# Performance work log

Measured on AMD Instinct MI355X. Metric: run time of the kernel, lower is better.

## Reference

```python
import jax, jax.numpy as jnp
import numpy as np

LEAK = 0.2
NUM_GRAPHS = 64


def _gat(h_in, src, dst, eh, W, att_src, att_dst, att_edge, lin_edge_W, bias, N):
    # PyG GATConv with edge_dim, concat=False (mean over heads)
    H, C = att_src.shape
    h = (h_in @ W).reshape(N, H, C)                      # [N,H,C]
    e = (eh @ lin_edge_W).reshape(-1, H, C)              # [Eaug,H,C]
    a_s = jnp.einsum('nhc,hc->nh', h, att_src)           # [N,H]
    a_d = jnp.einsum('nhc,hc->nh', h, att_dst)
    a_e = jnp.einsum('ehc,hc->eh', e, att_edge)          # [Eaug,H]
    score = jax.nn.leaky_relu(a_s[src] + a_d[dst] + a_e, LEAK)
    # scatter-softmax over incoming edges of each destination node
    m = jax.ops.segment_max(score, dst, num_segments=N)
    ex = jnp.exp(score - m[dst])
    den = jax.ops.segment_sum(ex, dst, num_segments=N)
    alpha = ex / den[dst]                                # [Eaug,H]
    out = jax.ops.segment_sum(alpha[:, :, None] * h[src], dst, num_segments=N)
    return out.mean(axis=1) + bias                       # concat=False -> head mean


def setup_inputs() -> dict:
    key = jax.random.key(0)
    ks = jax.random.split(key, 32)
    N, E, F, FE, HID, H, NT = 30000, 480000, 64, 16, 64, 4, 16
    Cin1 = F + HID
    s = 0.05
    d = {
        'x': jax.random.normal(ks[0], (N, F), jnp.float32),
        'edge_attr': jax.random.normal(ks[1], (E, FE), jnp.float32),
        'node_emb': jax.random.normal(ks[2], (NT, HID), jnp.float32) * s,
        'edge_W': jax.random.normal(ks[3], (FE, HID), jnp.float32) * s,
        'edge_b': jnp.zeros((HID,), jnp.float32),
        'W1': jax.random.normal(ks[4], (Cin1, H * HID), jnp.float32) * s,
        'as1': jax.random.normal(ks[5], (H, HID), jnp.float32) * s,
        'ad1': jax.random.normal(ks[6], (H, HID), jnp.float32) * s,
        'ae1': jax.random.normal(ks[7], (H, HID), jnp.float32) * s,
        'leW1': jax.random.normal(ks[8], (HID, H * HID), jnp.float32) * s,
        'b1': jnp.zeros((HID,), jnp.float32),
        'W2': jax.random.normal(ks[9], (HID, H * HID), jnp.float32) * s,
        'as2': jax.random.normal(ks[10], (H, HID), jnp.float32) * s,
        'ad2': jax.random.normal(ks[11], (H, HID), jnp.float32) * s,
        'ae2': jax.random.normal(ks[12], (H, HID), jnp.float32) * s,
        'leW2': jax.random.normal(ks[13], (HID, H * HID), jnp.float32) * s,
        'b2': jnp.zeros((HID,), jnp.float32),
        'sage_Wl': jax.random.normal(ks[14], (HID, HID), jnp.float32) * s,
        'sage_bl': jnp.zeros((HID,), jnp.float32),
        'sage_Wr': jax.random.normal(ks[15], (HID, HID), jnp.float32) * s,
        'lin1_W': jax.random.normal(ks[16], (HID, HID), jnp.float32) * s,
        'lin1_b': jnp.zeros((HID,), jnp.float32),
        'lin2_W': jax.random.normal(ks[17], (HID, HID), jnp.float32) * s,
        'lin2_b': jnp.zeros((HID,), jnp.float32),
        'tel_W': jax.random.normal(ks[18], (HID, 1), jnp.float32) * s,
        'tel_b': jnp.zeros((1,), jnp.float32),
        'comp_W': jax.random.normal(ks[19], (HID, 1), jnp.float32) * s,
        'comp_b': jnp.zeros((1,), jnp.float32),
        'pch_W': jax.random.normal(ks[20], (HID, 1), jnp.float32) * s,
        'pch_b': jnp.zeros((1,), jnp.float32),
        'edge_index': jax.random.randint(ks[21], (2, E), 0, N, jnp.int32),
        'batch': jnp.sort(jax.random.randint(ks[22], (N,), 0, NUM_GRAPHS, jnp.int32)),
        'node_type': jax.random.randint(ks[23], (N,), 0, NT, jnp.int32),
    }
    return d


def reference(x, edge_attr, node_emb, edge_W, edge_b,
              W1, as1, ad1, ae1, leW1, b1,
              W2, as2, ad2, ae2, leW2, b2,
              sage_Wl, sage_bl, sage_Wr,
              lin1_W, lin1_b, lin2_W, lin2_b,
              tel_W, tel_b, comp_W, comp_b, pch_W, pch_b,
              edge_index, batch, node_type):
    N = x.shape[0]
    src0, dst0 = edge_index[0], edge_index[1]

    h0 = jnp.concatenate([x, node_emb[node_type]], axis=-1)   # [N, F+HID]
    eh = edge_attr @ edge_W + edge_b                          # [E, HID]

    # GATConv default add_self_loops=True, fill_value='mean' on edge_attr
    loop = jnp.arange(N, dtype=src0.dtype)
    src = jnp.concatenate([src0, loop])
    dst = jnp.concatenate([dst0, loop])
    eh_aug = jnp.concatenate([eh, jnp.broadcast_to(eh.mean(axis=0), (N, eh.shape[1]))], axis=0)

    h1 = jax.nn.elu(_gat(h0, src, dst, eh_aug, W1, as1, ad1, ae1, leW1, b1, N))
    h2 = jax.nn.elu(_gat(h1, src, dst, eh_aug, W2, as2, ad2, ae2, leW2, b2, N))

    # SAGEConv: mean neighbor aggregation (src->dst) + root transform
    deg = jax.ops.segment_sum(jnp.ones_like(dst0, dtype=h2.dtype), dst0, num_segments=N)
    agg = jax.ops.segment_sum(h2[src0], dst0, num_segments=N) / jnp.clip(deg, 1.0)[:, None]
    h3 = jax.nn.elu(agg @ sage_Wl + sage_bl + h2 @ sage_Wr)

    # global mean pool per graph
    cnt = jax.ops.segment_sum(jnp.ones((N,), h3.dtype), batch, num_segments=NUM_GRAPHS)
    g = jax.ops.segment_sum(h3, batch, num_segments=NUM_GRAPHS) / jnp.clip(cnt, 1.0)[:, None]

    g = jax.nn.elu(g @ lin1_W + lin1_b)                       # dropout inactive (eval)
    g = g @ lin2_W + lin2_b
    return (g @ tel_W + tel_b, g @ comp_W + comp_b, g @ pch_W + pch_b)
```

## Files before the change

### kernel.cpp

```cpp
#include <hip/hip_runtime.h>
#include <math.h>

#define NN 30000
#define NE 480000
#define FEA 16
#define HID 64
#define NG 64
#define LEAKK 0.2f

#define S_MEANEA 0
#define S_AEL1   84
#define S_AEL2   156
#define S_MS1    160
#define S_MD1    672
#define S_MS2    1184
#define S_MD2    1440

__device__ __forceinline__ float eluf(float v) { return v > 0.f ? v : expm1f(v); }
__device__ __forceinline__ float leakyf(float v) { return v >= 0.f ? v : LEAKK * v; }
__device__ __forceinline__ void fma4(float4& a, float w, const float4& x) {
    a.x += w * x.x; a.y += w * x.y; a.z += w * x.z; a.w += w * x.w;
}
__device__ __forceinline__ unsigned bf16pack(float a, float b) {
    unsigned ua = __float_as_uint(a), ub = __float_as_uint(b);
    ua = (ua + 0x7FFFu + ((ua >> 16) & 1u)) >> 16;
    ub = (ub + 0x7FFFu + ((ub >> 16) & 1u)) >> 16;
    return ua | (ub << 16);
}
__device__ __forceinline__ uint2 bfpack4(float a, float b, float c, float d) {
    return make_uint2(bf16pack(a, b), bf16pack(c, d));
}
__device__ __forceinline__ float4 bf16x4(uint2 p) {
    float4 r;
    r.x = __uint_as_float(p.x << 16);
    r.y = __uint_as_float(p.x & 0xFFFF0000u);
    r.z = __uint_as_float(p.y << 16);
    r.w = __uint_as_float(p.y & 0xFFFF0000u);
    return r;
}
__device__ __forceinline__ float4 escore4(float4 a, float4 b, float4 c) {
    float4 r;
    r.x = expf(leakyf(a.x + b.x + c.x));
    r.y = expf(leakyf(a.y + b.y + c.y));
    r.z = expf(leakyf(a.z + b.z + c.z));
    r.w = expf(leakyf(a.w + b.w + c.w));
    return r;
}

__global__ __launch_bounds__(256) void cm_prepw_kernel(
    const int* __restrict__ dst, const float* __restrict__ EA,
    int* __restrict__ cnt, int* __restrict__ rank, float* __restrict__ S,
    const float* __restrict__ W1, const float* __restrict__ W2,
    const float* __restrict__ Wl, const float* __restrict__ Wr,
    const float* __restrict__ emb,
    const float* __restrict__ leW1, const float* __restrict__ aew1,
    const float* __restrict__ leW2, const float* __restrict__ aew2,
    const float* __restrict__ edge_W, const float* __restrict__ edge_b,
    float* __restrict__ WC1, float* __restrict__ WC2, float* __restrict__ B128,
    float* __restrict__ ae1s, float* __restrict__ ae2s) {
    int t = threadIdx.x;
    if (blockIdx.x < 176) {
        int i = blockIdx.x * 256 + t;
        if (i < 16384) {
            int hk = i >> 6, c = i & 63;
            int h = hk >> 6, k = hk & 63;
            WC1[i] = 0.25f * W1[k * 256 + h * 64 + c];
        } else if (i < 20480) {
            int j2 = i - 16384;
            int r2 = j2 >> 6, c = j2 & 63;
            int tau = r2 >> 2, h = r2 & 3;
            float v = 0.f;
            for (int j = 0; j < 64; j++)
                v += emb[tau * 64 + j] * W1[(64 + j) * 256 + h * 64 + c];
            WC1[i] = 0.25f * v;
        } else if (i < 36864) {
            int j = i - 20480;
            int hk = j >> 6, c = j & 63;
            int h = hk >> 6, k = hk & 63;
            WC2[j] = 0.25f * W2[k * 256 + h * 64 + c];
        } else if (i < 45056) {
            int j = i - 36864;
            int k = j >> 6, c = j & 63;
            B128[j] = (k < 64) ? Wl[k * 64 + c] : Wr[(k - 64) * 64 + c];
        }
        return;
    }
    __shared__ float M1s[256], M2s[256];
    __shared__ float KF1[64], KF2[64], C1s[4], C2s[4];
    __shared__ float wred[4][16];
    {
        int k = t >> 2, h = t & 3;
        float m1 = 0.f, m2 = 0.f;
        for (int c = 0; c < 64; c++) {
            m1 += leW1[k * 256 + h * 64 + c] * aew1[h * 64 + c];
            m2 += leW2[k * 256 + h * 64 + c] * aew2[h * 64 + c];
        }
        M1s[t] = m1; M2s[t] = m2;
    }
    __syncthreads();
    if (t < 64) {
        int f = t >> 2, h = t & 3;
        float k1 = 0.f, k2 = 0.f;
        for (int k = 0; k < 64; k++) {
            k1 += edge_W[f * 64 + k] * M1s[k * 4 + h];
            k2 += edge_W[f * 64 + k] * M2s[k * 4 + h];
        }
        KF1[t] = k1; KF2[t] = k2;
    } else if (t < 68) {
        int h = t - 64;
        float c1 = 0.f, c2 = 0.f;
        for (int k = 0; k < 64; k++) {
            c1 += edge_b[k] * M1s[k * 4 + h];
            c2 += edge_b[k] * M2s[k * 4 + h];
        }
        C1s[h] = c1; C2s[h] = c2;
    }
    __syncthreads();
    int base = (blockIdx.x - 176) * 512;
    float facc[16];
#pragma unroll
    for (int f = 0; f < 16; f++) facc[f] = 0.f;
#pragma unroll
    for (int i = 0; i < 2; i++) {
        int e = base + i * 256 + t;
        if (e < NE) {
            rank[e] = atomicAdd(&cnt[dst[e]], 1);
            float a1[4], a2[4];
#pragma unroll
            for (int h = 0; h < 4; h++) { a1[h] = C1s[h]; a2[h] = C2s[h]; }
            const float4* EA4 = (const float4*)(EA + (size_t)e * FEA);
#pragma unroll
            for (int q = 0; q < 4; q++) {
                float4 v = EA4[q];
                float vv[4] = {v.x, v.y, v.z, v.w};
#pragma unroll
                for (int j = 0; j < 4; j++) {
                    int f = q * 4 + j;
                    facc[f] += vv[j];
#pragma unroll
                    for (int h = 0; h < 4; h++) {
                        a1[h] += vv[j] * KF1[f * 4 + h];
                        a2[h] += vv[j] * KF2[f * 4 + h];
                    }
                }
            }
            ((float4*)ae1s)[e] = make_float4(a1[0], a1[1], a1[2], a1[3]);
            ((float4*)ae2s)[e] = make_float4(a2[0], a2[1], a2[2], a2[3]);
        }
    }
#pragma unroll
    for (int mask = 1; mask < 64; mask <<= 1) {
#pragma unroll
        for (int f = 0; f < 16; f++) facc[f] += __shfl_xor(facc[f], mask, 64);
    }
    int wid = t >> 6, lane = t & 63;
    if (lane == 0) {
#pragma unroll
        for (int f = 0; f < 16; f++) wred[wid][f] = facc[f];
    }
    __syncthreads();
    if (t < 16)
        atomicAdd(&S[S_MEANEA + t], wred[0][t] + wred[1][t] + wred[2][t] + wred[3][t]);
}

__global__ void scan_blocks_kernel(const int* __restrict__ cnt, int* __restrict__ eoff,
                                   int* __restrict__ bsum) {
    __shared__ int wsum[16];
    int t = threadIdx.x;
    int i = blockIdx.x * 1024 + t;
    int v = (i < NN) ? cnt[i] : 0;
    int lane = t & 63;
    int incl = v;
#pragma unroll
    for (int ofs = 1; ofs < 64; ofs <<= 1) {
        int u = __shfl_up(incl, ofs, 64);
        if (lane >= ofs) incl += u;
    }
    int wid = t >> 6;
    if (lane == 63) wsum[wid] = incl;
    __syncthreads();
    if (t < 16) {
        int s = wsum[t];
#pragma unroll
        for (int ofs = 1; ofs < 16; ofs <<= 1) {
            int u = __shfl_up(s, ofs, 64);
            if (t >= ofs) s += u;
        }
        wsum[t] = s;
    }
    __syncthreads();
    int excl = incl - v + (wid > 0 ? wsum[wid - 1] : 0);
    if (i < NN) eoff[i] = excl;
    if (t == 1023) bsum[blockIdx.x] = excl + v;
}

__global__ void tops_goff_prep_kernel(
    const int* __restrict__ bsum, int* __restrict__ boff, int nb,
    const int* __restrict__ batch, int* __restrict__ goff,
    const float* __restrict__ W1, const float* __restrict__ as1, const float* __restrict__ ad1,
    const float* __restrict__ ae1, const float* __restrict__ leW1,
    const float* __restrict__ W2, const float* __restrict__ as2, const float* __restrict__ ad2,
    const float* __restrict__ ae2, const float* __restrict__ leW2,
    const float* __restrict__ edge_W, const float* __restrict__ edge_b,
    float* __restrict__ S) {
    __shared__ float M1[256], M2[256], meh[64];
    int t = threadIdx.x;
    if (blockIdx.x == 0) {
        if (t >= 64) return;
        int v = (t < nb) ? bsum[t] : 0;
        int incl = v;
#pragma unroll
        for (int ofs = 1; ofs < 64; ofs <<= 1) {
            int u = __shfl_up(incl, ofs, 64);
            if (t >= ofs) incl += u;
        }
        boff[t] = incl - v;
        return;
    }
    if (blockIdx.x == 1) {
        if (t > NG) return;
        int lo = 0, hi = NN;
        while (lo < hi) {
            int mid = (lo + hi) >> 1;
            if (batch[mid] < t) lo = mid + 1; else hi = mid;
        }
        goff[t] = lo;
        return;
    }
    if (t < 16) S[S_MEANEA + t] *= (1.0f / (float)NE);
    __syncthreads();
    {
        int k = t >> 2, h = t & 3;
        float m1 = 0.f, m2 = 0.f;
        for (int c = 0; c < 64; c++) {
            m1 += leW1[k * 256 + h * 64 + c] * ae1[h * 64 + c];
            m2 += leW2[k * 256 + h * 64 + c] * ae2[h * 64 + c];
        }
        M1[t] = m1; M2[t] = m2;
    }
    if (t < 64) {
        float v = edge_b[t];
        for (int f = 0; f < FEA; f++) v += S[S_MEANEA + f] * edge_W[f * 64 + t];
        meh[t] = v;
    }
    __syncthreads();
    if (t >= 64 && t < 68) {
        int h = t - 64;
        float a1v = 0.f, a2v = 0.f;
        for (int k = 0; k < 64; k++) {
            a1v += meh[k] * M1[k * 4 + h];
            a2v += meh[k] * M2[k * 4 + h];
        }
        S[S_AEL1 + h] = a1v; S[S_AEL2 + h] = a2v;
    }
    for (int i = t; i < 512; i += 256) {
        int k = i >> 2, h = i & 3;
        float s = 0.f, d = 0.f;
        for (int c = 0; c < 64; c++) {
            float w = W1[k * 256 + h * 64 + c];
            s += w * as1[h * 64 + c];
            d += w * ad1[h * 64 + c];
        }
        S[S_MS1 + i] = s; S[S_MD1 + i] = d;
    }
    for (int i = t; i < 256; i += 256) {
        int k = i >> 2, h = i & 3;
        float s = 0.f, d = 0.f;
        for (int c = 0; c < 64; c++) {
            float w = W2[k * 256 + h * 64 + c];
            s += w * as2[h * 64 + c];
            d += w * ad2[h * 64 + c];
        }
        S[S_MS2 + i] = s; S[S_MD2 + i] = d;
    }
}

__global__ __launch_bounds__(256) void scanadd_attn_kernel(
    const int* __restrict__ boff, int* __restrict__ eoff,
    const float* __restrict__ x, const float* __restrict__ node_emb,
    const int* __restrict__ node_type, const float* __restrict__ S,
    float* __restrict__ as_, float* __restrict__ ad_, unsigned* __restrict__ xb) {
    __shared__ float xt[64 * 132];
    __shared__ float ms[512], md[512];
    __shared__ int ntS[64];
    int t = threadIdx.x;
    if (blockIdx.x < 118) {
        int i = blockIdx.x * 256 + t;
        if (i < NN) eoff[i] += boff[i >> 10];
        if (i == 0) eoff[NN] = NE;
        return;
    }
    int n0 = (blockIdx.x - 118) * 64;
    if (t < 64) {
        int n = n0 + t;
        ntS[t] = (n < NN) ? node_type[n] : 0;
    }
    for (int i = t; i < 512; i += 256) { ms[i] = S[S_MS1 + i]; md[i] = S[S_MD1 + i]; }
    __syncthreads();
    for (int i = t; i < 1024; i += 256) {
        int r = i >> 4, c4 = (i & 15) * 4;
        int n = n0 + r;
        float4 f = {0, 0, 0, 0};
        if (n < NN) f = *(const float4*)(x + (size_t)n * 64 + c4);
        *(float4*)&xt[r * 132 + c4] = f;
    }
    for (int i = t; i < 1024; i += 256) {
        int r = i >> 4, c4 = (i & 15) * 4;
        int n = n0 + r;
        float4 f = {0, 0, 0, 0};
        if (n < NN) f = *(const float4*)(node_emb + (size_t)ntS[r] * 64 + c4);
        *(float4*)&xt[r * 132 + 64 + c4] = f;
    }
    __syncthreads();
    for (int i = t; i < 2048; i += 256) {
        int r = i >> 5, u = i & 31;
        int n = n0 + r;
        if (n < NN)
            xb[(size_t)n * 32 + u] = bf16pack(xt[r * 132 + 2 * u], xt[r * 132 + 2 * u + 1]);
    }
    int r = t >> 2, h = t & 3;
    float s = 0.f, d = 0.f;
#pragma unroll 8
    for (int k = 0; k < 128; k++) {
        float xv = xt[r * 132 + k];
        s += xv * ms[k * 4 + h];
        d += xv * md[k * 4 + h];
    }
    int n = n0 + r;
    if (n < NN) { as_[n * 4 + h] = s; ad_[n * 4 + h] = d; }
}

__global__ __launch_bounds__(256) void scatter_score_kernel(
    const int* __restrict__ src, const int* __restrict__ dst,
    const float* __restrict__ ae1s,
    const float* __restrict__ as_, const float* __restrict__ ad_,
    const int* __restrict__ node_type,
    const int* __restrict__ eoff, const int* __restrict__ rank,
    int2* __restrict__ se_sorted, float* __restrict__ scs) {
    int e = blockIdx.x * 256 + threadIdx.x;
    if (e >= NE) return;
    int s = src[e], d = dst[e];
    float4 a1 = ((const float4*)ae1s)[e];
    float4 asv = ((const float4*)as_)[s];
    float4 adv = ((const float4*)ad_)[d];
    float4 r = escore4(asv, adv, a1);
    int pos = eoff[d] + rank[e];
    ((float4*)scs)[pos] = r;
    int ty = node_type[s];
    se_sorted[pos] = make_int2(s, e | (ty << 24));
}

__global__ __launch_bounds__(256) void agg_gat1_kernel(
    const int* __restrict__ eoff, const int2* __restrict__ se_sorted,
    const float* __restrict__ scs, const unsigned* __restrict__ xb,
    const int* __restrict__ node_type,
    const float* __restrict__ as_, const float* __restrict__ ad_,
    const float* __restrict__ Sael, uint2* __restrict__ aggb) {
    int n = blockIdx.x * 4 + (threadIdx.x >> 6);
    if (n >= NN) return;
    int lane = threadIdx.x & 63;
    int sub = lane >> 4, ch = lane & 15;
    const uint2* Xb = (const uint2*)xb;
    const float4* W4 = (const float4*)scs;
    float4 asn = ((const float4*)as_)[n];
    float4 adn = ((const float4*)ad_)[n];
    float4 a0 = {0, 0, 0, 0}, a1 = a0, a2 = a0, a3 = a0, dn = a0, tw = a0;
    int b = eoff[n], e_end = eoff[n + 1];
    int nE = e_end - b;
    int i = sub;
    for (; i + 4 < nE; i += 8) {
        int2 se0 = se_sorted[b + i], se1 = se_sorted[b + i + 4];
        int t0 = se0.y >> 24, t1 = se1.y >> 24;
        float4 w0 = W4[b + i], w1 = W4[b + i + 4];
        float4 x0 = bf16x4(Xb[(size_t)se0.x * 16 + ch]);
        float4 x1 = bf16x4(Xb[(size_t)se1.x * 16 + ch]);
        fma4(a0, w0.x, x0); fma4(a1, w0.y, x0); fma4(a2, w0.z, x0); fma4(a3, w0.w, x0);
        fma4(a0, w1.x, x1); fma4(a1, w1.y, x1); fma4(a2, w1.z, x1); fma4(a3, w1.w, x1);
        dn.x += w0.x + w1.x; dn.y += w0.y + w1.y;
        dn.z += w0.z + w1.z; dn.w += w0.w + w1.w;
        if (ch == t0) { tw.x += w0.x; tw.y += w0.y; tw.z += w0.z; tw.w += w0.w; }
        if (ch == t1) { tw.x += w1.x; tw.y += w1.y; tw.z += w1.z; tw.w += w1.w; }
    }
    for (; i < nE; i += 4) {
        int2 se0 = se_sorted[b + i];
        int t0 = se0.y >> 24;
        float4 w0 = W4[b + i];
        float4 x0 = bf16x4(Xb[(size_t)se0.x * 16 + ch]);
        fma4(a0, w0.x, x0); fma4(a1, w0.y, x0); fma4(a2, w0.z, x0); fma4(a3, w0.w, x0);
        dn.x += w0.x; dn.y += w0.y; dn.z += w0.z; dn.w += w0.w;
        if (ch == t0) { tw.x += w0.x; tw.y += w0.y; tw.z += w0.z; tw.w += w0.w; }
    }
    if (sub == 0) {
        float e0 = expf(leakyf(asn.x + adn.x + Sael[0]));
        float e1 = expf(leakyf(asn.y + adn.y + Sael[1]));
        float e2 = expf(leakyf(asn.z + adn.z + Sael[2]));
        float e3 = expf(leakyf(asn.w + adn.w + Sael[3]));
        float4 xs = bf16x4(Xb[(size_t)n * 16 + ch]);
        fma4(a0, e0, xs); fma4(a1, e1, xs); fma4(a2, e2, xs); fma4(a3, e3, xs);
        dn.x += e0; dn.y += e1; dn.z += e2; dn.w += e3;
        int tn = node_type[n];
        if (ch == tn) { tw.x += e0; tw.y += e1; tw.z += e2; tw.w += e3; }
    }
#pragma unroll
    for (int mask = 16; mask < 64; mask <<= 1) {
        a0.x += __shfl_xor(a0.x, mask, 64); a0.y += __shfl_xor(a0.y, mask, 64);
        a0.z += __shfl_xor(a0.z, mask, 64); a0.w += __shfl_xor(a0.w, mask, 64);
        a1.x += __shfl_xor(a1.x, mask, 64); a1.y += __shfl_xor(a1.y, mask, 64);
        a1.z += __shfl_xor(a1.z, mask, 64); a1.w += __shfl_xor(a1.w, mask, 64);
        a2.x += __shfl_xor(a2.x, mask, 64); a2.y += __shfl_xor(a2.y, mask, 64);
        a2.z += __shfl_xor(a2.z, mask, 64); a2.w += __shfl_xor(a2.w, mask, 64);
        a3.x += __shfl_xor(a3.x, mask, 64); a3.y += __shfl_xor(a3.y, mask, 64);
        a3.z += __shfl_xor(a3.z, mask, 64); a3.w += __shfl_xor(a3.w, mask, 64);
        dn.x += __shfl_xor(dn.x, mask, 64); dn.y += __shfl_xor(dn.y, mask, 64);
        dn.z += __shfl_xor(dn.z, mask, 64); dn.w += __shfl_xor(dn.w, mask, 64);
        tw.x += __shfl_xor(tw.x, mask, 64); tw.y += __shfl_xor(tw.y, mask, 64);
        tw.z += __shfl_xor(tw.z, mask, 64); tw.w += __shfl_xor(tw.w, mask, 64);
    }
    if (sub == 0) {
        float i0 = 1.f / dn.x, i1 = 1.f / dn.y, i2 = 1.f / dn.z, i3 = 1.f / dn.w;
        uint2* A2 = aggb + (size_t)n * 80;
        A2[ch]      = bfpack4(a0.x * i0, a0.y * i0, a0.z * i0, a0.w * i0);
        A2[16 + ch] = bfpack4(a1.x * i1, a1.y * i1, a1.z * i1, a1.w * i1);
        A2[32 + ch] = bfpack4(a2.x * i2, a2.y * i2, a2.z * i2, a2.w * i2);
        A2[48 + ch] = bfpack4(a3.x * i3, a3.y * i3, a3.z * i3, a3.w * i3);
        A2[64 + ch] = bfpack4(tw.x * i0, tw.y * i1, tw.z * i2, tw.w * i3);
    }
}

__global__ __launch_bounds__(256) void agg_gat2_kernel(
    const int* __restrict__ eoff, const int2* __restrict__ se_sorted,
    const float* __restrict__ ae2s, const unsigned* __restrict__ h1b,
    const float* __restrict__ as_, const float* __restrict__ ad_,
    const float* __restrict__ Sael, uint2* __restrict__ aggb) {
    int n = blockIdx.x * 4 + (threadIdx.x >> 6);
    if (n >= NN) return;
    int lane = threadIdx.x & 63;
    int sub = lane >> 4, ch = lane & 15;
    const uint2* Xb = (const uint2*)h1b;
    const float4* AE4 = (const float4*)ae2s;
    const float4* AS4 = (const float4*)as_;
    float4 asn = AS4[n];
    float4 adn = ((const float4*)ad_)[n];
    float4 a0 = {0, 0, 0, 0}, a1 = a0, a2 = a0, a3 = a0, dn = a0;
    int b = eoff[n], e = eoff[n + 1];
    int nE = e - b;
    int i = sub;
    for (; i + 4 < nE; i += 8) {
        int2 se0 = se_sorted[b + i], se1 = se_sorted[b + i + 4];
        int e0 = se0.y & 0xFFFFFF, e1 = se1.y & 0xFFFFFF;
        float4 q0 = AE4[e0], q1 = AE4[e1];
        float4 s0 = AS4[se0.x], s1 = AS4[se1.x];
        float4 x0 = bf16x4(Xb[(size_t)se0.x * 16 + ch]);
        float4 x1 = bf16x4(Xb[(size_t)se1.x * 16 + ch]);
        float4 w0 = escore4(s0, adn, q0);
        float4 w1 = escore4(s1, adn, q1);
        fma4(a0, w0.x, x0); fma4(a1, w0.y, x0); fma4(a2, w0.z, x0); fma4(a3, w0.w, x0);
        fma4(a0, w1.x, x1); fma4(a1, w1.y, x1); fma4(a2, w1.z, x1); fma4(a3, w1.w, x1);
        dn.x += w0.x + w1.x; dn.y += w0.y + w1.y;
        dn.z += w0.z + w1.z; dn.w += w0.w + w1.w;
    }
    for (; i < nE; i += 4) {
        int2 se0 = se_sorted[b + i];
        int e0 = se0.y & 0xFFFFFF;
        float4 w0 = escore4(AS4[se0.x], adn, AE4[e0]);
        float4 x0 = bf16x4(Xb[(size_t)se0.x * 16 + ch]);
        fma4(a0, w0.x, x0); fma4(a1, w0.y, x0); fma4(a2, w0.z, x0); fma4(a3, w0.w, x0);
        dn.x += w0.x; dn.y += w0.y; dn.z += w0.z; dn.w += w0.w;
    }
    if (sub == 0) {
        float e0 = expf(leakyf(asn.x + adn.x + Sael[0]));
        float e1 = expf(leakyf(asn.y + adn.y + Sael[1]));
        float e2 = expf(leakyf(asn.z + adn.z + Sael[2]));
        float e3 = expf(leakyf(asn.w + adn.w + Sael[3]));
        float4 xs = bf16x4(Xb[(size_t)n * 16 + ch]);
        fma4(a0, e0, xs); fma4(a1, e1, xs); fma4(a2, e2, xs); fma4(a3, e3, xs);
        dn.x += e0; dn.y += e1; dn.z += e2; dn.w += e3;
    }
#pragma unroll
    for (int mask = 16; mask < 64; mask <<= 1) {
        a0.x += __shfl_xor(a0.x, mask, 64); a0.y += __shfl_xor(a0.y, mask, 64);
        a0.z += __shfl_xor(a0.z, mask, 64); a0.w += __shfl_xor(a0.w, mask, 64);
        a1.x += __shfl_xor(a1.x, mask, 64); a1.y += __shfl_xor(a1.y, mask, 64);
        a1.z += __shfl_xor(a1.z, mask, 64); a1.w += __shfl_xor(a1.w, mask, 64);
        a2.x += __shfl_xor(a2.x, mask, 64); a2.y += __shfl_xor(a2.y, mask, 64);
        a2.z += __shfl_xor(a2.z, mask, 64); a2.w += __shfl_xor(a2.w, mask, 64);
        a3.x += __shfl_xor(a3.x, mask, 64); a3.y += __shfl_xor(a3.y, mask, 64);
        a3.z += __shfl_xor(a3.z, mask, 64); a3.w += __shfl_xor(a3.w, mask, 64);
        dn.x += __shfl_xor(dn.x, mask, 64); dn.y += __shfl_xor(dn.y, mask, 64);
        dn.z += __shfl_xor(dn.z, mask, 64); dn.w += __shfl_xor(dn.w, mask, 64);
    }
    if (sub == 0) {
        float i0 = 1.f / dn.x, i1 = 1.f / dn.y, i2 = 1.f / dn.z, i3 = 1.f / dn.w;
        uint2* A2 = aggb + (size_t)n * 64;
        A2[ch]      = bfpack4(a0.x * i0, a0.y * i0, a0.z * i0, a0.w * i0);
        A2[16 + ch] = bfpack4(a1.x * i1, a1.y * i1, a1.z * i1, a1.w * i1);
        A2[32 + ch] = bfpack4(a2.x * i2, a2.y * i2, a2.z * i2, a2.w * i2);
// ... 121 lines not shown
#pragma unroll
                for (int h = 0; h < 4; h++) {
                    ps[i][h] += __shfl_xor(ps[i][h], mk, 64);
                    pd[i][h] += __shfl_xor(pd[i][h], mk, 64);
                }
        }
        if (tx == 0) {
#pragma unroll
            for (int i = 0; i < 4; i++) {
                int m = m_base + ty * 4 + i;
                if (m < NN) {
                    *(float4*)(as_ + (size_t)m * 4) =
                        make_float4(ps[i][0], ps[i][1], ps[i][2], ps[i][3]);
                    *(float4*)(ad_ + (size_t)m * 4) =
                        make_float4(pd[i][0], pd[i][1], pd[i][2], pd[i][3]);
                }
            }
        }
    }
}

__global__ __launch_bounds__(256) void sage_agg3_kernel(
    const unsigned* __restrict__ h2b,
    const int* __restrict__ eoff, const int2* __restrict__ se_sorted,
    uint2* __restrict__ AB) {
    int n = blockIdx.x * 16 + (threadIdx.x >> 4);
    if (n >= NN) return;
    int l = threadIdx.x & 15;
    const uint2* Hb = (const uint2*)h2b;
    float ax = 0.f, ay = 0.f, az = 0.f, aw = 0.f;
    int b = eoff[n], e_end = eoff[n + 1];
    int idx = b;
    int stop = b + ((e_end - b) & ~7);
    if (idx < stop) {
        int sreg[8];
#pragma unroll
        for (int u = 0; u < 8; u++) sreg[u] = se_sorted[idx + u].x;
        idx += 8;
        while (true) {
            int sn[8];
            bool more = idx < stop;
            if (more) {
#pragma unroll
                for (int u = 0; u < 8; u++) sn[u] = se_sorted[idx + u].x;
            }
#pragma unroll
            for (int u = 0; u < 8; u++) {
                float4 v = bf16x4(Hb[(size_t)sreg[u] * 16 + l]);
                ax += v.x; ay += v.y; az += v.z; aw += v.w;
            }
            if (!more) break;
#pragma unroll
            for (int u = 0; u < 8; u++) sreg[u] = sn[u];
            idx += 8;
        }
    }
    for (; idx < e_end; idx++) {
        float4 v0 = bf16x4(Hb[(size_t)se_sorted[idx].x * 16 + l]);
        ax += v0.x; ay += v0.y; az += v0.z; aw += v0.w;
    }
    float dg = (float)(e_end - b);
    if (dg < 1.f) dg = 1.f;
    float inv = 1.f / dg;
    AB[(size_t)n * 32 + l] = bfpack4(ax * inv, ay * inv, az * inv, aw * inv);
    AB[(size_t)n * 32 + 16 + l] = Hb[(size_t)n * 16 + l];
}

__global__ __launch_bounds__(256) void pool_mlp_kernel(
    const float* __restrict__ h3, const int* __restrict__ goff,
    const float* __restrict__ lin1W, const float* __restrict__ lin1b,
    const float* __restrict__ lin2W, const float* __restrict__ lin2b,
    const float* __restrict__ telW, const float* __restrict__ telb,
    const float* __restrict__ compW, const float* __restrict__ compb,
    const float* __restrict__ pchW, const float* __restrict__ pchb,
    float* __restrict__ out) {
    __shared__ float red[256];
    __shared__ float g[64], G1[64], G2[64];
    int gi = blockIdx.x, t = threadIdx.x;
    int c = t & 63, li = t >> 6;
    int b = goff[gi], e = goff[gi + 1];
    float sum = 0.f;
// ... 80 lines not shown
    float* outp = (float*)d_out;

    const int* srcp = edge_index;
    const int* dstp = edge_index + NE;

    float* wf = (float*)d_ws;
    constexpr size_t OFF_H3    = 0;
    constexpr size_t OFF_AGG   = OFF_H3 + (size_t)NN * 64;
    constexpr size_t OFF_AE1   = OFF_AGG + (size_t)NN * 512;
    constexpr size_t OFF_H2    = OFF_AE1 + (size_t)NE * 4;
    constexpr size_t OFF_SC    = OFF_H2 + (size_t)NN * 64;
    constexpr size_t OFF_AE2   = OFF_SC + (size_t)NE * 4;
    constexpr size_t OFF_AS    = OFF_AE2 + (size_t)NE * 4;
    constexpr size_t OFF_AD    = OFF_AS + (size_t)NN * 4;
    constexpr size_t OFF_SMALL = OFF_AD + (size_t)NN * 4;
    constexpr size_t OFF_WC1   = OFF_SMALL + 4096;
    constexpr size_t OFF_WC2   = OFF_WC1 + 20480;
    constexpr size_t OFF_B128  = OFF_WC2 + 16384;
    constexpr size_t OFF_XB    = OFF_B128 + 8192;
    constexpr size_t OFF_H1B   = OFF_XB + (size_t)NN * 32;
    constexpr size_t OFF_H2B   = OFF_H1B + (size_t)NN * 32;
    constexpr size_t F_TOTAL   = OFF_H2B + (size_t)NN * 32;

    int* wi         = (int*)(wf + F_TOTAL);
    int* cnt        = wi;
    int* rank       = wi + NN;
    int* eoff       = rank + NE;
    int2* se_sorted = (int2*)(eoff + (NN + 2));
    int* goff       = (int*)(se_sorted + NE);
    int* bsum       = goff + (NG + 1);
    int* boff       = bsum + 64;

    float* h3    = wf + OFF_H3;
    float* aggb  = wf + OFF_AGG;
    float* ae1s  = wf + OFF_AE1;
    float* sc    = wf + OFF_SC;
    float* ae2s  = wf + OFF_AE2;
    float* as_   = wf + OFF_AS;
    float* ad_   = wf + OFF_AD;
    float* S     = wf + OFF_SMALL;
    float* WC1   = wf + OFF_WC1;
    float* WC2   = wf + OFF_WC2;
    float* B128  = wf + OFF_B128;
    unsigned* xb  = (unsigned*)(wf + OFF_XB);
    unsigned* h1b = (unsigned*)(wf + OFF_H1B);
    unsigned* h2b = (unsigned*)(wf + OFF_H2B);

    hipMemsetAsync(S + S_MEANEA, 0, 16 * sizeof(float), stream);
    hipMemsetAsync(cnt, 0, NN * sizeof(int), stream);

    cm_prepw_kernel<<<176 + (NE + 511) / 512, 256, 0, stream>>>(
        dstp, EA, cnt, rank, S, W1, W2, sage_Wl, sage_Wr, node_emb,
        leW1, ae1, leW2, ae2, edge_W, edge_b, WC1, WC2, B128, ae1s, ae2s);
    {
        int nb = (NN + 1023) / 1024;
        scan_blocks_kernel<<<nb, 1024, 0, stream>>>(cnt, eoff, bsum);
        tops_goff_prep_kernel<<<3, 256, 0, stream>>>(
            bsum, boff, nb, batch, goff,
            W1, as1, ad1, ae1, leW1, W2, as2, ad2, ae2, leW2, edge_W, edge_b, S);
        scanadd_attn_kernel<<<118 + (NN + 63) / 64, 256, 0, stream>>>(
            boff, eoff, x, node_emb, node_type, S, as_, ad_, xb);
    }
    scatter_score_kernel<<<(NE + 255) / 256, 256, 0, stream>>>(
        srcp, dstp, ae1s, as_, ad_, node_type, eoff, rank, se_sorted, sc);

    agg_gat1_kernel<<<(NN + 3) / 4, 256, 0, stream>>>(
        eoff, se_sorted, sc, xb, node_type, as_, ad_, S + S_AEL1, (uint2*)aggb);
    gemm64_kernel<320, true><<<(NN + 63) / 64, 256, 0, stream>>>(
        (const unsigned*)aggb, WC1, b1, nullptr, h1b, S + S_MS2, S + S_MD2, as_, ad_);

    agg_gat2_kernel<<<(NN + 3) / 4, 256, 0, stream>>>(
        eoff, se_sorted, ae2s, h1b, as_, ad_, S + S_AEL2, (uint2*)aggb);
    gemm64_kernel<256, false><<<(NN + 63) / 64, 256, 0, stream>>>(
        (const unsigned*)aggb, WC2, b2, nullptr, h2b, nullptr, nullptr, nullptr, nullptr);

    sage_agg3_kernel<<<(NN + 15) / 16, 256, 0, stream>>>(h2b, eoff, se_sorted, (uint2*)aggb);
    gemm64_kernel<128, false><<<(NN + 63) / 64, 256, 0, stream>>>(
        (const unsigned*)aggb, B128, sage_bl, h3, nullptr, nullptr, nullptr, nullptr, nullptr);

    pool_mlp_kernel<<<NG, 256, 0, stream>>>(h3, goff, lin1_W, lin1_b, lin2_W, lin2_b,
                                            tel_W, tel_b, comp_W, comp_b, pch_W, pch_b, outp);
}
```

Before: 407.4 us.

## Restructure preprocessing: compute edge projections in dst-sorted order and fuse tiny prep kernels

The per-edge attention-edge projection moves from the counting kernel into the scatter kernel, which writes ae1/ae2 directly in destination-sorted order. The GAT1 aggregation now computes the edge scores on the fly, the same way GAT2 already did. The self-loop mean term is derived by summing the projected values rather than the raw edge attributes. The small prep kernel is folded into extra blocks of the first kernel and the block-offset scan is recomputed inline, which removes a launch. The sorted index shrinks from int2 to a packed int of 16-bit source plus type, so aggregation reads are sequential and narrower. In exchange, exp work moves into GAT1 aggregation, and the packing assumes node ids and types fit in 16 bits.

```diff
diff --git a/kernel.cpp b/kernel.cpp
--- a/kernel.cpp
+++ b/kernel.cpp
@@ -8,9 +8,12 @@
 #define NG 64
 #define LEAKK 0.2f
 
-#define S_MEANEA 0
-#define S_AEL1   84
-#define S_AEL2   156
+#define S_AEL1   0
+#define S_AEL2   4
+#define S_KF1    16
+#define S_C1     80
+#define S_KF2    88
+#define S_C2     152
 #define S_MS1    160
 #define S_MD1    672
 #define S_MS2    1184
@@ -48,19 +51,21 @@
 }
 
 __global__ __launch_bounds__(256) void cm_prepw_kernel(
-    const int* __restrict__ dst, const float* __restrict__ EA,
-    int* __restrict__ cnt, int* __restrict__ rank, float* __restrict__ S,
+    const int* __restrict__ dst, int* __restrict__ cnt, int* __restrict__ rank,
     const float* __restrict__ W1, const float* __restrict__ W2,
     const float* __restrict__ Wl, const float* __restrict__ Wr,
     const float* __restrict__ emb,
     const float* __restrict__ leW1, const float* __restrict__ aew1,
     const float* __restrict__ leW2, const float* __restrict__ aew2,
     const float* __restrict__ edge_W, const float* __restrict__ edge_b,
+    const float* __restrict__ as1, const float* __restrict__ ad1,
+    const float* __restrict__ as2, const float* __restrict__ ad2,
+    const int* __restrict__ batch,
     float* __restrict__ WC1, float* __restrict__ WC2, float* __restrict__ B128,
-    float* __restrict__ ae1s, float* __restrict__ ae2s) {
-    int t = threadIdx.x;
-    if (blockIdx.x < 176) {
-        int i = blockIdx.x * 256 + t;
+    float* __restrict__ S, int* __restrict__ goff) {
+    int t = threadIdx.x, bx = blockIdx.x;
+    if (bx < 176) {
+        int i = bx * 256 + t;
         if (i < 16384) {
             int hk = i >> 6, c = i & 63;
             int h = hk >> 6, k = hk & 63;
@@ -85,82 +90,72 @@
         }
         return;
     }
-    __shared__ float M1s[256], M2s[256];
-    __shared__ float KF1[64], KF2[64], C1s[4], C2s[4];
-    __shared__ float wred[4][16];
-    {
+    if (bx < 178) {
+        int i = (bx - 176) * 256 + t;
+        int k = i >> 2, h = i & 3;
+        float s = 0.f, d = 0.f;
+        for (int c = 0; c < 64; c++) {
+            float w = W1[k * 256 + h * 64 + c];
+            s += w * as1[h * 64 + c];
+            d += w * ad1[h * 64 + c];
+        }
+        S[S_MS1 + i] = s; S[S_MD1 + i] = d;
+        return;
+    }
+    if (bx == 178) {
         int k = t >> 2, h = t & 3;
-        float m1 = 0.f, m2 = 0.f;
+        float s = 0.f, d = 0.f;
         for (int c = 0; c < 64; c++) {
-            m1 += leW1[k * 256 + h * 64 + c] * aew1[h * 64 + c];
-            m2 += leW2[k * 256 + h * 64 + c] * aew2[h * 64 + c];
-        }
-        M1s[t] = m1; M2s[t] = m2;
-    }
-    __syncthreads();
-    if (t < 64) {
-        int f = t >> 2, h = t & 3;
-        float k1 = 0.f, k2 = 0.f;
-        for (int k = 0; k < 64; k++) {
-            k1 += edge_W[f * 64 + k] * M1s[k * 4 + h];
-            k2 += edge_W[f * 64 + k] * M2s[k * 4 + h];
-        }
-        KF1[t] = k1; KF2[t] = k2;
-    } else if (t < 68) {
-        int h = t - 64;
-        float c1 = 0.f, c2 = 0.f;
-        for (int k = 0; k < 64; k++) {
-            c1 += edge_b[k] * M1s[k * 4 + h];
-            c2 += edge_b[k] * M2s[k * 4 + h];
-        }
-        C1s[h] = c1; C2s[h] = c2;
-    }
-    __syncthreads();
-    int base = (blockIdx.x - 176) * 512;
-    float facc[16];
-#pragma unroll
-    for (int f = 0; f < 16; f++) facc[f] = 0.f;
-#pragma unroll
-    for (int i = 0; i < 2; i++) {
-        int e = base + i * 256 + t;
-        if (e < NE) {
-            rank[e] = atomicAdd(&cnt[dst[e]], 1);
-            float a1[4], a2[4];
-#pragma unroll
-            for (int h = 0; h < 4; h++) { a1[h] = C1s[h]; a2[h] = C2s[h]; }
-            const float4* EA4 = (const float4*)(EA + (size_t)e * FEA);
-#pragma unroll
-            for (int q = 0; q < 4; q++) {
-                float4 v = EA4[q];
-                float vv[4] = {v.x, v.y, v.z, v.w};
-#pragma unroll
-                for (int j = 0; j < 4; j++) {
-                    int f = q * 4 + j;
-                    facc[f] += vv[j];
-#pragma unroll
-                    for (int h = 0; h < 4; h++) {
-                        a1[h] += vv[j] * KF1[f * 4 + h];
-                        a2[h] += vv[j] * KF2[f * 4 + h];
-                    }
-                }
+            float w = W2[k * 256 + h * 64 + c];
+            s += w * as2[h * 64 + c];
+            d += w * ad2[h * 64 + c];
+        }
+        S[S_MS2 + t] = s; S[S_MD2 + t] = d;
+        return;
+    }
+    if (bx == 179) {
+        __shared__ float M1s[256], M2s[256];
+        {
+            int k = t >> 2, h = t & 3;
+            float m1 = 0.f, m2 = 0.f;
+            for (int c = 0; c < 64; c++) {
+                m1 += leW1[k * 256 + h * 64 + c] * aew1[h * 64 + c];
+                m2 += leW2[k * 256 + h * 64 + c] * aew2[h * 64 + c];
             }
-            ((float4*)ae1s)[e] = make_float4(a1[0], a1[1], a1[2], a1[3]);
-            ((float4*)ae2s)[e] = make_float4(a2[0], a2[1], a2[2], a2[3]);
-        }
-    }
-#pragma unroll
-    for (int mask = 1; mask < 64; mask <<= 1) {
-#pragma unroll
-        for (int f = 0; f < 16; f++) facc[f] += __shfl_xor(facc[f], mask, 64);
-    }
-    int wid = t >> 6, lane = t & 63;
-    if (lane == 0) {
-#pragma unroll
-        for (int f = 0; f < 16; f++) wred[wid][f] = facc[f];
-    }
-    __syncthreads();
-    if (t < 16)
-        atomicAdd(&S[S_MEANEA + t], wred[0][t] + wred[1][t] + wred[2][t] + wred[3][t]);
+            M1s[t] = m1; M2s[t] = m2;
+        }
+        __syncthreads();
+        if (t < 64) {
+            int f = t >> 2, h = t & 3;
+            float k1 = 0.f, k2 = 0.f;
+            for (int k = 0; k < 64; k++) {
+                k1 += edge_W[f * 64 + k] * M1s[k * 4 + h];
+                k2 += edge_W[f * 64 + k] * M2s[k * 4 + h];
+            }
+            S[S_KF1 + t] = k1; S[S_KF2 + t] = k2;
+        } else if (t < 68) {
+            int h = t - 64;
+            float c1 = 0.f, c2 = 0.f;
+            for (int k = 0; k < 64; k++) {
+                c1 += edge_b[k] * M1s[k * 4 + h];
+                c2 += edge_b[k] * M2s[k * 4 + h];
+            }
+            S[S_C1 + h] = c1; S[S_C2 + h] = c2;
+        }
+        return;
+    }
+    if (bx == 180) {
+        if (t > NG) return;
+        int lo = 0, hi = NN;
+        while (lo < hi) {
+            int mid = (lo + hi) >> 1;
+            if (batch[mid] < t) lo = mid + 1; else hi = mid;
+        }
+        goff[t] = lo;
+        return;
+    }
+    int e = (bx - 181) * 256 + t;
+    if (e < NE) rank[e] = atomicAdd(&cnt[dst[e]], 1);
 }
 
 __global__ void scan_blocks_kernel(const int* __restrict__ cnt, int* __restrict__ eoff,
@@ -194,89 +189,8 @@
     if (t == 1023) bsum[blockIdx.x] = excl + v;
 }
 
-__global__ void tops_goff_prep_kernel(
-    const int* __restrict__ bsum, int* __restrict__ boff, int nb,
-    const int* __restrict__ batch, int* __restrict__ goff,
-    const float* __restrict__ W1, const float* __restrict__ as1, const float* __restrict__ ad1,
-    const float* __restrict__ ae1, const float* __restrict__ leW1,
-    const float* __restrict__ W2, const float* __restrict__ as2, const float* __restrict__ ad2,
-    const float* __restrict__ ae2, const float* __restrict__ leW2,
-    const float* __restrict__ edge_W, const float* __restrict__ edge_b,
-    float* __restrict__ S) {
-    __shared__ float M1[256], M2[256], meh[64];
-    int t = threadIdx.x;
-    if (blockIdx.x == 0) {
-        if (t >= 64) return;
-        int v = (t < nb) ? bsum[t] : 0;
-        int incl = v;
-#pragma unroll
-        for (int ofs = 1; ofs < 64; ofs <<= 1) {
-            int u = __shfl_up(incl, ofs, 64);
-            if (t >= ofs) incl += u;
-        }
-        boff[t] = incl - v;
-        return;
-    }
-    if (blockIdx.x == 1) {
-        if (t > NG) return;
-        int lo = 0, hi = NN;
-        while (lo < hi) {
-            int mid = (lo + hi) >> 1;
-            if (batch[mid] < t) lo = mid + 1; else hi = mid;
-        }
-        goff[t] = lo;
-        return;
-    }
-    if (t < 16) S[S_MEANEA + t] *= (1.0f / (float)NE);
-    __syncthreads();
-    {
-        int k = t >> 2, h = t & 3;
-        float m1 = 0.f, m2 = 0.f;
-        for (int c = 0; c < 64; c++) {
-            m1 += leW1[k * 256 + h * 64 + c] * ae1[h * 64 + c];
-            m2 += leW2[k * 256 + h * 64 + c] * ae2[h * 64 + c];
-        }
-        M1[t] = m1; M2[t] = m2;
-    }
-    if (t < 64) {
-        float v = edge_b[t];
-        for (int f = 0; f < FEA; f++) v += S[S_MEANEA + f] * edge_W[f * 64 + t];
-        meh[t] = v;
-    }
-    __syncthreads();
-    if (t >= 64 && t < 68) {
-        int h = t - 64;
-        float a1v = 0.f, a2v = 0.f;
-        for (int k = 0; k < 64; k++) {
-            a1v += meh[k] * M1[k * 4 + h];
-            a2v += meh[k] * M2[k * 4 + h];
-        }
-        S[S_AEL1 + h] = a1v; S[S_AEL2 + h] = a2v;
-    }
-    for (int i = t; i < 512; i += 256) {
-        int k = i >> 2, h = i & 3;
-        float s = 0.f, d = 0.f;
-        for (int c = 0; c < 64; c++) {
-            float w = W1[k * 256 + h * 64 + c];
-            s += w * as1[h * 64 + c];
-            d += w * ad1[h * 64 + c];
-        }
-        S[S_MS1 + i] = s; S[S_MD1 + i] = d;
-    }
-    for (int i = t; i < 256; i += 256) {
-        int k = i >> 2, h = i & 3;
-        float s = 0.f, d = 0.f;
-        for (int c = 0; c < 64; c++) {
-            float w = W2[k * 256 + h * 64 + c];
-            s += w * as2[h * 64 + c];
-            d += w * ad2[h * 64 + c];
-        }
-        S[S_MS2 + i] = s; S[S_MD2 + i] = d;
-    }
-}
-
 __global__ __launch_bounds__(256) void scanadd_attn_kernel(
-    const int* __restrict__ boff, int* __restrict__ eoff,
+    const int* __restrict__ bsum, int* __restrict__ eoff,
     const float* __restrict__ x, const float* __restrict__ node_emb,
     const int* __restrict__ node_type, const float* __restrict__ S,
     float* __restrict__ as_, float* __restrict__ ad_, unsigned* __restrict__ xb) {
@@ -285,8 +199,11 @@
     __shared__ int ntS[64];
     int t = threadIdx.x;
     if (blockIdx.x < 118) {
+        int j = blockIdx.x >> 2;
+        int pref = 0;
+        for (int u = 0; u < j; u++) pref += bsum[u];
         int i = blockIdx.x * 256 + t;
-        if (i < NN) eoff[i] += boff[i >> 10];
+        if (i < NN) eoff[i] += pref;
         if (i == 0) eoff[NN] = NE;
         return;
     }
@@ -330,50 +247,84 @@
     if (n < NN) { as_[n * 4 + h] = s; ad_[n * 4 + h] = d; }
 }
 
-__global__ __launch_bounds__(256) void scatter_score_kernel(
+__global__ __launch_bounds__(256) void scatter_proj_kernel(
     const int* __restrict__ src, const int* __restrict__ dst,
-    const float* __restrict__ ae1s,
-    const float* __restrict__ as_, const float* __restrict__ ad_,
+    const float* __restrict__ EA, const float* __restrict__ S,
     const int* __restrict__ node_type,
     const int* __restrict__ eoff, const int* __restrict__ rank,
-    int2* __restrict__ se_sorted, float* __restrict__ scs) {
-    int e = blockIdx.x * 256 + threadIdx.x;
-    if (e >= NE) return;
+    int* __restrict__ sep, float4* __restrict__ ae1st, float4* __restrict__ ae2st,
+    float* __restrict__ Ssum) {
+    __shared__ float KF1s[64], KF2s[64], Cs[8];
+    __shared__ float red[32];
+    int t = threadIdx.x;
+    if (t < 64) { KF1s[t] = S[S_KF1 + t]; KF2s[t] = S[S_KF2 + t]; }
+    else if (t < 72) { int q = t - 64; Cs[q] = (q < 4) ? S[S_C1 + q] : S[S_C2 + q - 4]; }
+    __syncthreads();
+    int e = blockIdx.x * 256 + t;
     int s = src[e], d = dst[e];
-    float4 a1 = ((const float4*)ae1s)[e];
-    float4 asv = ((const float4*)as_)[s];
-    float4 adv = ((const float4*)ad_)[d];
-    float4 r = escore4(asv, adv, a1);
+    float a1[4], a2[4];
+#pragma unroll
+    for (int h = 0; h < 4; h++) { a1[h] = Cs[h]; a2[h] = Cs[4 + h]; }
+    const float4* EA4 = (const float4*)(EA + (size_t)e * FEA);
+#pragma unroll
+    for (int q = 0; q < 4; q++) {
+        float4 v = EA4[q];
+        float vv[4] = {v.x, v.y, v.z, v.w};
+#pragma unroll
+        for (int j = 0; j < 4; j++) {
+            int f = q * 4 + j;
+#pragma unroll
+            for (int h = 0; h < 4; h++) {
+                a1[h] += vv[j] * KF1s[f * 4 + h];
+                a2[h] += vv[j] * KF2s[f * 4 + h];
+            }
+        }
+    }
     int pos = eoff[d] + rank[e];
-    ((float4*)scs)[pos] = r;
-    int ty = node_type[s];
-    se_sorted[pos] = make_int2(s, e | (ty << 24));
+    sep[pos] = s | (node_type[s] << 16);
+    ae1st[pos] = make_float4(a1[0], a1[1], a1[2], a1[3]);
+    ae2st[pos] = make_float4(a2[0], a2[1], a2[2], a2[3]);
+    float v[8] = {a1[0], a1[1], a1[2], a1[3], a2[0], a2[1], a2[2], a2[3]};
+#pragma unroll
+    for (int mask = 1; mask < 64; mask <<= 1)
+#pragma unroll
+        for (int j = 0; j < 8; j++) v[j] += __shfl_xor(v[j], mask, 64);
+    int lane = t & 63, wid = t >> 6;
+    if (lane == 0)
+#pragma unroll
+        for (int j = 0; j < 8; j++) red[wid * 8 + j] = v[j];
+    __syncthreads();
+    if (t < 8) atomicAdd(&Ssum[t], red[t] + red[8 + t] + red[16 + t] + red[24 + t]);
 }
 
 __global__ __launch_bounds__(256) void agg_gat1_kernel(
-    const int* __restrict__ eoff, const int2* __restrict__ se_sorted,
-    const float* __restrict__ scs, const unsigned* __restrict__ xb,
+    const int* __restrict__ eoff, const int* __restrict__ sep,
+    const float* __restrict__ ae1st, const unsigned* __restrict__ xb,
     const int* __restrict__ node_type,
     const float* __restrict__ as_, const float* __restrict__ ad_,
-    const float* __restrict__ Sael, uint2* __restrict__ aggb) {
+    const float* __restrict__ S, uint2* __restrict__ aggb) {
     int n = blockIdx.x * 4 + (threadIdx.x >> 6);
     if (n >= NN) return;
     int lane = threadIdx.x & 63;
     int sub = lane >> 4, ch = lane & 15;
     const uint2* Xb = (const uint2*)xb;
-    const float4* W4 = (const float4*)scs;
-    float4 asn = ((const float4*)as_)[n];
+    const float4* AE4 = (const float4*)ae1st;
+    const float4* AS4 = (const float4*)as_;
+    float4 asn = AS4[n];
     float4 adn = ((const float4*)ad_)[n];
     float4 a0 = {0, 0, 0, 0}, a1 = a0, a2 = a0, a3 = a0, dn = a0, tw = a0;
     int b = eoff[n], e_end = eoff[n + 1];
     int nE = e_end - b;
     int i = sub;
     for (; i + 4 < nE; i += 8) {
-        int2 se0 = se_sorted[b + i], se1 = se_sorted[b + i + 4];
-        int t0 = se0.y >> 24, t1 = se1.y >> 24;
-        float4 w0 = W4[b + i], w1 = W4[b + i + 4];
-        float4 x0 = bf16x4(Xb[(size_t)se0.x * 16 + ch]);
-        float4 x1 = bf16x4(Xb[(size_t)se1.x * 16 + ch]);
+        int p0 = b + i, p1 = p0 + 4;
+        int q0 = sep[p0], q1 = sep[p1];
+        int s0 = q0 & 0xFFFF, t0 = q0 >> 16;
+        int s1 = q1 & 0xFFFF, t1 = q1 >> 16;
+        float4 w0 = escore4(AS4[s0], adn, AE4[p0]);
+        float4 w1 = escore4(AS4[s1], adn, AE4[p1]);
+        float4 x0 = bf16x4(Xb[(size_t)s0 * 16 + ch]);
+        float4 x1 = bf16x4(Xb[(size_t)s1 * 16 + ch]);
         fma4(a0, w0.x, x0); fma4(a1, w0.y, x0); fma4(a2, w0.z, x0); fma4(a3, w0.w, x0);
         fma4(a0, w1.x, x1); fma4(a1, w1.y, x1); fma4(a2, w1.z, x1); fma4(a3, w1.w, x1);
         dn.x += w0.x + w1.x; dn.y += w0.y + w1.y;
@@ -382,19 +333,21 @@
         if (ch == t1) { tw.x += w1.x; tw.y += w1.y; tw.z += w1.z; tw.w += w1.w; }
     }
     for (; i < nE; i += 4) {
-        int2 se0 = se_sorted[b + i];
-        int t0 = se0.y >> 24;
-        float4 w0 = W4[b + i];
-        float4 x0 = bf16x4(Xb[(size_t)se0.x * 16 + ch]);
+        int p0 = b + i;
+        int q0 = sep[p0];
+        int s0 = q0 & 0xFFFF, t0 = q0 >> 16;
+        float4 w0 = escore4(AS4[s0], adn, AE4[p0]);
+        float4 x0 = bf16x4(Xb[(size_t)s0 * 16 + ch]);
         fma4(a0, w0.x, x0); fma4(a1, w0.y, x0); fma4(a2, w0.z, x0); fma4(a3, w0.w, x0);
         dn.x += w0.x; dn.y += w0.y; dn.z += w0.z; dn.w += w0.w;
         if (ch == t0) { tw.x += w0.x; tw.y += w0.y; tw.z += w0.z; tw.w += w0.w; }
     }
     if (sub == 0) {
-        float e0 = expf(leakyf(asn.x + adn.x + Sael[0]));
-        float e1 = expf(leakyf(asn.y + adn.y + Sael[1]));
-        float e2 = expf(leakyf(asn.z + adn.z + Sael[2]));
-        float e3 = expf(leakyf(asn.w + adn.w + Sael[3]));
+        const float inv = 1.f / (float)NE;
+        float e0 = expf(leakyf(asn.x + adn.x + S[S_AEL1 + 0] * inv));
+        float e1 = expf(leakyf(asn.y + adn.y + S[S_AEL1 + 1] * inv));
+        float e2 = expf(leakyf(asn.z + adn.z + S[S_AEL1 + 2] * inv));
+        float e3 = expf(leakyf(asn.w + adn.w + S[S_AEL1 + 3] * inv));
         float4 xs = bf16x4(Xb[(size_t)n * 16 + ch]);
         fma4(a0, e0, xs); fma4(a1, e1, xs); fma4(a2, e2, xs); fma4(a3, e3, xs);
         dn.x += e0; dn.y += e1; dn.z += e2; dn.w += e3;
@@ -428,16 +381,16 @@
 }
 
 __global__ __launch_bounds__(256) void agg_gat2_kernel(
-    const int* __restrict__ eoff, const int2* __restrict__ se_sorted,
-    const float* __restrict__ ae2s, const unsigned* __restrict__ h1b,
+    const int* __restrict__ eoff, const int* __restrict__ sep,
+    const float* __restrict__ ae2st, const unsigned* __restrict__ h1b,
     const float* __restrict__ as_, const float* __restrict__ ad_,
-    const float* __restrict__ Sael, uint2* __restrict__ aggb) {
+    const float* __restrict__ S, uint2* __restrict__ aggb) {
     int n = blockIdx.x * 4 + (threadIdx.x >> 6);
     if (n >= NN) return;
     int lane = threadIdx.x & 63;
     int sub = lane >> 4, ch = lane & 15;
     const uint2* Xb = (const uint2*)h1b;
-    const float4* AE4 = (const float4*)ae2s;
+    const float4* AE4 = (const float4*)ae2st;
     const float4* AS4 = (const float4*)as_;
     float4 asn = AS4[n];
     float4 adn = ((const float4*)ad_)[n];
@@ -446,32 +399,33 @@
     int nE = e - b;
     int i = sub;
     for (; i + 4 < nE; i += 8) {
-        int2 se0 = se_sorted[b + i], se1 = se_sorted[b + i + 4];
-        int e0 = se0.y & 0xFFFFFF, e1 = se1.y & 0xFFFFFF;
-        float4 q0 = AE4[e0], q1 = AE4[e1];
-        float4 s0 = AS4[se0.x], s1 = AS4[se1.x];
-        float4 x0 = bf16x4(Xb[(size_t)se0.x * 16 + ch]);
-        float4 x1 = bf16x4(Xb[(size_t)se1.x * 16 + ch]);
-        float4 w0 = escore4(s0, adn, q0);
-        float4 w1 = escore4(s1, adn, q1);
+        int p0 = b + i, p1 = p0 + 4;
+        int q0 = sep[p0], q1 = sep[p1];
+        int s0 = q0 & 0xFFFF, s1 = q1 & 0xFFFF;
+        float4 w0 = escore4(AS4[s0], adn, AE4[p0]);
+        float4 w1 = escore4(AS4[s1], adn, AE4[p1]);
+        float4 x0 = bf16x4(Xb[(size_t)s0 * 16 + ch]);
+        float4 x1 = bf16x4(Xb[(size_t)s1 * 16 + ch]);
         fma4(a0, w0.x, x0); fma4(a1, w0.y, x0); fma4(a2, w0.z, x0); fma4(a3, w0.w, x0);
         fma4(a0, w1.x, x1); fma4(a1, w1.y, x1); fma4(a2, w1.z, x1); fma4(a3, w1.w, x1);
         dn.x += w0.x + w1.x; dn.y += w0.y + w1.y;
         dn.z += w0.z + w1.z; dn.w += w0.w + w1.w;
     }
     for (; i < nE; i += 4) {
-        int2 se0 = se_sorted[b + i];
-        int e0 = se0.y & 0xFFFFFF;
-        float4 w0 = escore4(AS4[se0.x], adn, AE4[e0]);
-        float4 x0 = bf16x4(Xb[(size_t)se0.x * 16 + ch]);
+        int p0 = b + i;
+        int q0 = sep[p0];
+        int s0 = q0 & 0xFFFF;
+        float4 w0 = escore4(AS4[s0], adn, AE4[p0]);
+        float4 x0 = bf16x4(Xb[(size_t)s0 * 16 + ch]);
         fma4(a0, w0.x, x0); fma4(a1, w0.y, x0); fma4(a2, w0.z, x0); fma4(a3, w0.w, x0);
         dn.x += w0.x; dn.y += w0.y; dn.z += w0.z; dn.w += w0.w;
     }
     if (sub == 0) {
-        float e0 = expf(leakyf(asn.x + adn.x + Sael[0]));
-        float e1 = expf(leakyf(asn.y + adn.y + Sael[1]));
-        float e2 = expf(leakyf(asn.z + adn.z + Sael[2]));
-        float e3 = expf(leakyf(asn.w + adn.w + Sael[3]));
+        const float inv = 1.f / (float)NE;
+        float e0 = expf(leakyf(asn.x + adn.x + S[S_AEL2 + 0] * inv));
+        float e1 = expf(leakyf(asn.y + adn.y + S[S_AEL2 + 1] * inv));
+        float e2 = expf(leakyf(asn.z + adn.z + S[S_AEL2 + 2] * inv));
+        float e3 = expf(leakyf(asn.w + adn.w + S[S_AEL2 + 3] * inv));
         float4 xs = bf16x4(Xb[(size_t)n * 16 + ch]);
         fma4(a0, e0, xs); fma4(a1, e1, xs); fma4(a2, e2, xs); fma4(a3, e3, xs);
         dn.x += e0; dn.y += e1; dn.z += e2; dn.w += e3;
@@ -639,7 +593,7 @@
 
 __global__ __launch_bounds__(256) void sage_agg3_kernel(
     const unsigned* __restrict__ h2b,
-    const int* __restrict__ eoff, const int2* __restrict__ se_sorted,
+    const int* __restrict__ eoff, const int* __restrict__ sep,
     uint2* __restrict__ AB) {
     int n = blockIdx.x * 16 + (threadIdx.x >> 4);
     if (n >= NN) return;
@@ -652,14 +606,14 @@
     if (idx < stop) {
         int sreg[8];
 #pragma unroll
-        for (int u = 0; u < 8; u++) sreg[u] = se_sorted[idx + u].x;
+        for (int u = 0; u < 8; u++) sreg[u] = sep[idx + u] & 0xFFFF;
         idx += 8;
         while (true) {
             int sn[8];
             bool more = idx < stop;
             if (more) {
 #pragma unroll
-                for (int u = 0; u < 8; u++) sn[u] = se_sorted[idx + u].x;
+                for (int u = 0; u < 8; u++) sn[u] = sep[idx + u] & 0xFFFF;
             }
 #pragma unroll
             for (int u = 0; u < 8; u++) {
@@ -673,7 +627,7 @@
         }
     }
     for (; idx < e_end; idx++) {
-        float4 v0 = bf16x4(Hb[(size_t)se_sorted[idx].x * 16 + l]);
+        float4 v0 = bf16x4(Hb[(size_t)(sep[idx] & 0xFFFF) * 16 + l]);
         ax += v0.x; ay += v0.y; az += v0.z; aw += v0.w;
     }
     float dg = (float)(e_end - b);
@@ -800,20 +754,18 @@
     constexpr size_t OFF_H2B   = OFF_H1B + (size_t)NN * 32;
     constexpr size_t F_TOTAL   = OFF_H2B + (size_t)NN * 32;
 
-    int* wi         = (int*)(wf + F_TOTAL);
-    int* cnt        = wi;
-    int* rank       = wi + NN;
-    int* eoff       = rank + NE;
-    int2* se_sorted = (int2*)(eoff + (NN + 2));
-    int* goff       = (int*)(se_sorted + NE);
-    int* bsum       = goff + (NG + 1);
-    int* boff       = bsum + 64;
+    int* wi   = (int*)(wf + F_TOTAL);
+    int* cnt  = wi;
+    int* rank = wi + NN;
+    int* eoff = rank + NE;
+    int* sep  = eoff + (NN + 2);
+    int* goff = sep + NE;
+    int* bsum = goff + (NG + 1);
 
     float* h3    = wf + OFF_H3;
     float* aggb  = wf + OFF_AGG;
-    float* ae1s  = wf + OFF_AE1;
-    float* sc    = wf + OFF_SC;
-    float* ae2s  = wf + OFF_AE2;
+    float* ae1st = wf + OFF_AE1;
+    float* ae2st = wf + OFF_AE2;
     float* as_   = wf + OFF_AS;
     float* ad_   = wf + OFF_AD;
     float* S     = wf + OFF_SMALL;
@@ -824,35 +776,33 @@
     unsigned* h1b = (unsigned*)(wf + OFF_H1B);
     unsigned* h2b = (unsigned*)(wf + OFF_H2B);
 
-    hipMemsetAsync(S + S_MEANEA, 0, 16 * sizeof(float), stream);
+    hipMemsetAsync(S, 0, 16 * sizeof(float), stream);
     hipMemsetAsync(cnt, 0, NN * sizeof(int), stream);
 
-    cm_prepw_kernel<<<176 + (NE + 511) / 512, 256, 0, stream>>>(
-        dstp, EA, cnt, rank, S, W1, W2, sage_Wl, sage_Wr, node_emb,
-        leW1, ae1, leW2, ae2, edge_W, edge_b, WC1, WC2, B128, ae1s, ae2s);
-    {
-        int nb = (NN + 1023) / 1024;
-        scan_blocks_kernel<<<nb, 1024, 0, stream>>>(cnt, eoff, bsum);
-        tops_goff_prep_kernel<<<3, 256, 0, stream>>>(
-            bsum, boff, nb, batch, goff,
-            W1, as1, ad1, ae1, leW1, W2, as2, ad2, ae2, leW2, edge_W, edge_b, S);
-        scanadd_attn_kernel<<<118 + (NN + 63) / 64, 256, 0, stream>>>(
-            boff, eoff, x, node_emb, node_type, S, as_, ad_, xb);
-    }
-    scatter_score_kernel<<<(NE + 255) / 256, 256, 0, stream>>>(
-        srcp, dstp, ae1s, as_, ad_, node_type, eoff, rank, se_sorted, sc);
+    cm_prepw_kernel<<<181 + (NE + 255) / 256, 256, 0, stream>>>(
+        dstp, cnt, rank, W1, W2, sage_Wl, sage_Wr, node_emb,
+        leW1, ae1, leW2, ae2, edge_W, edge_b, as1, ad1, as2, ad2, batch,
+        WC1, WC2, B128, S, goff);
+
+    scan_blocks_kernel<<<(NN + 1023) / 1024, 1024, 0, stream>>>(cnt, eoff, bsum);
+    scanadd_attn_kernel<<<118 + (NN + 63) / 64, 256, 0, stream>>>(
+        bsum, eoff, x, node_emb, node_type, S, as_, ad_, xb);
+
+    scatter_proj_kernel<<<NE / 256, 256, 0, stream>>>(
+        srcp, dstp, EA, S, node_type, eoff, rank,
+        sep, (float4*)ae1st, (float4*)ae2st, S);
 
     agg_gat1_kernel<<<(NN + 3) / 4, 256, 0, stream>>>(
-        eoff, se_sorted, sc, xb, node_type, as_, ad_, S + S_AEL1, (uint2*)aggb);
+        eoff, sep, ae1st, xb, node_type, as_, ad_, S, (uint2*)aggb);
     gemm64_kernel<320, true><<<(NN + 63) / 64, 256, 0, stream>>>(
         (const unsigned*)aggb, WC1, b1, nullptr, h1b, S + S_MS2, S + S_MD2, as_, ad_);
 
     agg_gat2_kernel<<<(NN + 3) / 4, 256, 0, stream>>>(
-        eoff, se_sorted, ae2s, h1b, as_, ad_, S + S_AEL2, (uint2*)aggb);
+        eoff, sep, ae2st, h1b, as_, ad_, S, (uint2*)aggb);
     gemm64_kernel<256, false><<<(NN + 63) / 64, 256, 0, stream>>>(
         (const unsigned*)aggb, WC2, b2, nullptr, h2b, nullptr, nullptr, nullptr, nullptr);
 
-    sage_agg3_kernel<<<(NN + 15) / 16, 256, 0, stream>>>(h2b, eoff, se_sorted, (uint2*)aggb);
+    sage_agg3_kernel<<<(NN + 15) / 16, 256, 0, stream>>>(h2b, eoff, sep, (uint2*)aggb);
     gemm64_kernel<128, false><<<(NN + 63) / 64, 256, 0, stream>>>(
         (const unsigned*)aggb, B128, sage_bl, h3, nullptr, nullptr, nullptr, nullptr, nullptr);
 
```

Result: no change. 407.0 us (-0.1%).
